# Optimization experiments

Measured on AMD Instinct MI355X. Metric: run time of the kernel, lower is better.

The kernel has to match this reference:

```python
import jax, jax.numpy as jnp
import numpy as np

B, T, D, H, DK, DV, C, M = 8, 512, 1024, 8, 128, 128, 512, 512
TAU = float(DK) ** 0.5

def _ln(x, g, b, eps=1e-6):
    mu = x.mean(-1, keepdims=True)
    var = ((x - mu) ** 2).mean(-1, keepdims=True)
    return (x - mu) * jax.lax.rsqrt(var + eps) * g + b

def _hln(x, eps=1e-6):
    mu = x.mean(-1, keepdims=True)
    var = ((x - mu) ** 2).mean(-1, keepdims=True)
    return (x - mu) * jax.lax.rsqrt(var + eps)

def setup_inputs() -> dict:
    key = jax.random.key(0)
    ks = jax.random.split(key, 14)
    s = lambda k, shape, fan: jax.random.normal(k, shape, jnp.float32) * (fan ** -0.5)
    return {
        "x": jax.random.normal(ks[0], (B, T, D), jnp.float32),
        "doc_ids": jax.random.randint(ks[1], (B, T), 0, 4),
        "loss_mask": jnp.ones((B, T), jnp.float32),
        "xl_k_hat": jax.random.normal(ks[2], (B, H, M, DK), jnp.float32),
        "xl_v": jax.random.normal(ks[3], (B, H, M, DV), jnp.float32),
        "agg_upper": jax.random.normal(ks[4], (B, H, C, DV), jnp.float32),
        "agg_lower": jax.random.uniform(ks[5], (B, H, C), jnp.float32) * 8.0,
        "w_ln_g": jnp.ones((D,), jnp.float32),
        "w_ln_b": jnp.zeros((D,), jnp.float32),
        "w_q": s(ks[6], (D, H * DK), D),
        "w_k": s(ks[7], (D, H * DK), D),
        "w_v": s(ks[8], (D, H * DV), D),
        "w_g": s(ks[9], (D, H * DV), D),
        "w_res": s(ks[10], (H * DV, D), H * DV),
        "x_u": jax.random.normal(ks[11], (H, DK), jnp.float32) * 0.02,
        "codebook": jax.random.normal(ks[12], (H, C, DK), jnp.float32),
    }

def reference(x, doc_ids, loss_mask, xl_k_hat, xl_v, agg_upper, agg_lower,
              w_ln_g, w_ln_b, w_q, w_k, w_v, w_g, w_res, x_u, codebook):
    # ---- compute_k_q_v_g ----
    xt = _ln(x, w_ln_g, w_ln_b)                                  # [B,T,D]
    q = _hln((xt @ w_q).reshape(B, T, H, DK).transpose(0, 2, 1, 3))  # [B,H,T,DK]
    k = _hln((xt @ w_k).reshape(B, T, H, DK).transpose(0, 2, 1, 3))  # [B,H,T,DK]
    v = (xt @ w_v).reshape(B, T, H, DV).transpose(0, 2, 1, 3)        # [B,H,T,DV]
    g = jax.nn.silu(xt @ w_g)                                        # [B,T,H*DV]

    # ---- vector quantize keys (LearnableVQ) ----
    # dist[b,h,t,c] = ||k - codebook||^2 ; argmin -> shortcodes z
    kc = jnp.einsum('bhtd,hcd->bhtc', k, codebook)
    dist = (k ** 2).sum(-1)[..., None] - 2.0 * kc + (codebook ** 2).sum(-1)[None, :, None, :]
    z = jnp.argmin(dist, axis=-1)                                 # [B,H,T] shortcodes
    k_hat = codebook[jnp.arange(H)[None, :, None], z]             # [B,H,T,DK]
    k_hat_st = k + jax.lax.stop_gradient(k_hat - k)               # straight-through
    mask = loss_mask[:, None, :]                                  # [B,1,T]
    denom_m = mask.sum() * H + 1e-6
    l_commit = (((k - jax.lax.stop_gradient(k_hat)) ** 2).sum(-1) * mask).sum() / denom_m
    l_codebook = (((jax.lax.stop_gradient(k) - k_hat) ** 2).sum(-1) * mask).sum() / denom_m

    # ---- attention over xlcache ++ present, plus aggregated codeword cache ----
    recent_k = jnp.concatenate([xl_k_hat, k_hat_st], axis=2)      # [B,H,M+T,DK]
    recent_v = jnp.concatenate([xl_v, v], axis=2)                 # [B,H,M+T,DV]
    qb = q + x_u[None, :, None, :]
    s_rec = jnp.einsum('bhtd,bhsd->bhts', qb, recent_k) / TAU     # [B,H,T,M+T]
    s_agg = jnp.einsum('bhtd,hcd->bhtc', qb, codebook) / TAU      # [B,H,T,C]

    i = jnp.arange(T)[:, None]
    j = jnp.arange(M + T)[None, :]
    allow = ((j - M) <= i).astype(s_rec.dtype)                    # causal over recent window
    NEG = jnp.asarray(-1e30, s_rec.dtype)
    s_rec_m = jnp.where(allow > 0, s_rec, NEG)

    m = jnp.maximum(s_rec_m.max(-1), s_agg.max(-1))               # [B,H,T]
    a_rec = jnp.exp(s_rec_m - m[..., None]) * allow               # [B,H,T,M+T]
    a_agg = jnp.exp(s_agg - m[..., None])                         # [B,H,T,C]
    den = a_rec.sum(-1) + jnp.einsum('bhtc,bhc->bht', a_agg, agg_lower)
    num = (jnp.einsum('bhts,bhsd->bhtd', a_rec, recent_v)
           + jnp.einsum('bhtc,bhcd->bhtd', a_agg, agg_upper))
    wv = num / den[..., None]                                     # [B,H,T,DV]

    o = wv.transpose(0, 2, 1, 3).reshape(B, T, H * DV) * g        # gated
    res = o @ w_res                                               # [B,T,D]
    return res, l_commit, l_codebook
```

## Files before the change

kernel.cpp:

```cpp
#include <hip/hip_runtime.h>
#include <math.h>

namespace {

constexpr int nB = 8, nT = 512, nD = 1024, nH = 8, nDK = 128, nDV = 128, nC = 512, nM = 512;
constexpr int NROW = nB * nT;
constexpr float RTAU = 0.08838834764831845f;

typedef __attribute__((ext_vector_type(8))) short short8;
typedef __attribute__((ext_vector_type(4))) float f32x4;

__device__ __forceinline__ ushort f2bf(float f) {
  union { float f; uint u; } x; x.f = f;
  uint r = x.u + 0x7fff + ((x.u >> 16) & 1);
  return (ushort)(r >> 16);
}
__device__ __forceinline__ uint pk2(float a, float b) {
  return (uint)f2bf(a) | ((uint)f2bf(b) << 16);
}
__device__ __forceinline__ float bf2f(ushort u) {
  return __uint_as_float(((uint)u) << 16);
}
__device__ __forceinline__ void gload16(const void* g, void* l) {
  __builtin_amdgcn_global_load_lds((const __attribute__((address_space(1))) void*)g,
                                   (__attribute__((address_space(3))) void*)l, 16, 0, 0);
}

__device__ __forceinline__ float blockReduce256(float v, float* sm) {
  int lane = threadIdx.x & 63, w = threadIdx.x >> 6;
#pragma unroll
  for (int off = 32; off; off >>= 1) v += __shfl_down(v, off);
  if (lane == 0) sm[w] = v;
  __syncthreads();
  float r = sm[0] + sm[1] + sm[2] + sm[3];
  __syncthreads();
  return r;
}

__global__ __launch_bounds__(256) void ln_kernel(const float* __restrict__ x,
                                                 const float* __restrict__ gw,
                                                 const float* __restrict__ bw,
                                                 ushort* __restrict__ xt_bf) {
  __shared__ float sm[4];
  size_t row = blockIdx.x;
  float4 v = ((const float4*)(x + row * nD))[threadIdx.x];
  float mu = blockReduce256(v.x + v.y + v.z + v.w, sm) * (1.f / nD);
  float4 d = make_float4(v.x - mu, v.y - mu, v.z - mu, v.w - mu);
  float var = blockReduce256(d.x * d.x + d.y * d.y + d.z * d.z + d.w * d.w, sm) * (1.f / nD);
  float rs = rsqrtf(var + 1e-6f);
  float4 gg = ((const float4*)gw)[threadIdx.x];
  float4 bb = ((const float4*)bw)[threadIdx.x];
  float4 o = make_float4(d.x * rs * gg.x + bb.x, d.y * rs * gg.y + bb.y,
                         d.z * rs * gg.z + bb.z, d.w * rs * gg.w + bb.w);
  uint2 pb;
  pb.x = pk2(o.x, o.y);
  pb.y = pk2(o.z, o.w);
  ((uint2*)(xt_bf + row * nD))[threadIdx.x] = pb;
}

__global__ __launch_bounds__(256) void tobf3_kernel(const float* __restrict__ s0,
                                                    ushort* __restrict__ d0,
                                                    const float* __restrict__ s1,
                                                    ushort* __restrict__ d1,
                                                    const float* __restrict__ s2,
                                                    ushort* __restrict__ d2) {
  const float* src = blockIdx.y == 0 ? s0 : (blockIdx.y == 1 ? s1 : s2);
  ushort* dst = blockIdx.y == 0 ? d0 : (blockIdx.y == 1 ? d1 : d2);
  size_t i = (size_t)blockIdx.x * 256 + threadIdx.x;
  float4 v = ((const float4*)src)[i];
  uint2 p;
  p.x = pk2(v.x, v.y);
  p.y = pk2(v.z, v.w);
  ((uint2*)dst)[i] = p;
}

__global__ __launch_bounds__(256) void wtrans_kernel(const float* __restrict__ wq,
                                                     const float* __restrict__ wk,
                                                     const float* __restrict__ wv,
                                                     const float* __restrict__ wg,
                                                     const float* __restrict__ wres,
                                                     ushort* __restrict__ wqkvg_t,
                                                     ushort* __restrict__ wres_t) {
  __shared__ float tile[64][65];
  const int kz = blockIdx.x * 64;
  const int nz = blockIdx.y * 64;
  const float* W;
  ushort* D;
  if (blockIdx.z == 0)      { W = wq;   D = wqkvg_t; }
  else if (blockIdx.z == 1) { W = wk;   D = wqkvg_t + (size_t)1024 * 1024; }
  else if (blockIdx.z == 2) { W = wv;   D = wqkvg_t + (size_t)2048 * 1024; }
  else if (blockIdx.z == 3) { W = wg;   D = wqkvg_t + (size_t)3072 * 1024; }
  else                      { W = wres; D = wres_t; }
  const int c = threadIdx.x & 63, r4 = threadIdx.x >> 6;
#pragma unroll
  for (int i = 0; i < 16; ++i) {
    int r = i * 4 + r4;
    tile[r][c] = W[(size_t)(kz + r) * 1024 + nz + c];
  }
  __syncthreads();
#pragma unroll
  for (int i = 0; i < 16; ++i) {
    int n = i * 4 + r4;
    D[(size_t)(nz + n) * 1024 + kz + c] = f2bf(tile[c][n]);
  }
}

template <int MODE>
__global__ __launch_bounds__(256) void gemm_bf16_kernel(const ushort* __restrict__ A,
                                                        const ushort* __restrict__ Bt,
                                                        float* __restrict__ C0,
                                                        ushort* __restrict__ C1,
                                                        ushort* __restrict__ C2,
                                                        ushort* __restrict__ C3) {
  __shared__ __align__(16) ushort As[128 * 32];
  __shared__ __align__(16) ushort Bs[128 * 32];
  const int tid = threadIdx.x;
  const int w = tid >> 6, l = tid & 63;
  const int lr = l & 15, lg = l >> 4;
  const int wr = w >> 1, wc = w & 1;
  const int n0 = blockIdx.x * 128;
  const int m0 = blockIdx.y * 128;
  constexpr int K = 1024;

  f32x4 acc[4][4];
#pragma unroll
  for (int i = 0; i < 4; ++i)
#pragma unroll
    for (int j = 0; j < 4; ++j) acc[i][j] = (f32x4){0.f, 0.f, 0.f, 0.f};

  const int e0 = w * 512 + l * 8;
  const int r0 = e0 >> 5, c0 = e0 & 31;
  const int e1 = 2048 + e0;
  const int r1 = e1 >> 5, c1 = e1 & 31;
  const ushort* a0p = A + (size_t)(m0 + r0) * K + c0;
  const ushort* a1p = A + (size_t)(m0 + r1) * K + c1;
  const ushort* b0p = Bt + (size_t)(n0 + r0) * K + c0;
  const ushort* b1p = Bt + (size_t)(n0 + r1) * K + c1;
  ushort* lA0 = &As[w * 512];
  ushort* lA1 = &As[2048 + w * 512];
  ushort* lB0 = &Bs[w * 512];
  ushort* lB1 = &Bs[2048 + w * 512];

  for (int k0 = 0; k0 < K; k0 += 32) {
    __syncthreads();
    gload16(a0p + k0, lA0);
    gload16(a1p + k0, lA1);
    gload16(b0p + k0, lB0);
    gload16(b1p + k0, lB1);
    __syncthreads();
    short8 af[4], bfr[4];
#pragma unroll
    for (int i = 0; i < 4; ++i) af[i] = *(const short8*)&As[(wr * 64 + i * 16 + lr) * 32 + lg * 8];
#pragma unroll
    for (int j = 0; j < 4; ++j) bfr[j] = *(const short8*)&Bs[(wc * 64 + j * 16 + lr) * 32 + lg * 8];
    __builtin_amdgcn_s_setprio(1);
#pragma unroll
    for (int i = 0; i < 4; ++i)
#pragma unroll
      for (int j = 0; j < 4; ++j)
        acc[i][j] = __builtin_amdgcn_mfma_f32_16x16x32_bf16(af[i], bfr[j], acc[i][j], 0, 0, 0);
    __builtin_amdgcn_s_setprio(0);
  }

  const int seg = n0 >> 10;
  const int nbase = n0 & 1023;
#pragma unroll
  for (int i = 0; i < 4; ++i)
#pragma unroll
    for (int j = 0; j < 4; ++j)
#pragma unroll
      for (int r2 = 0; r2 < 4; ++r2) {
        const int row = m0 + wr * 64 + i * 16 + lg * 4 + r2;
        const int col = wc * 64 + j * 16 + lr;
        float v = acc[i][j][r2];
        if (MODE == 0) {
          C0[(size_t)row * 1024 + n0 + col] = v;
        } else {
          const int nloc = nbase + col;
          if (seg == 0)      C1[(size_t)row * 1024 + nloc] = f2bf(v);
          else if (seg == 1) C0[(size_t)row * 1024 + nloc] = v;
          else if (seg == 2) C2[(size_t)row * 1024 + nloc] = f2bf(v);
          else {
            float s = v / (1.f + __expf(-v));
            C3[(size_t)row * 1024 + nloc] = f2bf(s);
          }
        }
      }
}

__global__ __launch_bounds__(256) void hln_kernel(float* __restrict__ buf,
                                                  ushort* __restrict__ kbf,
                                                  float* __restrict__ knorm2) {
  int lane = threadIdx.x & 63;
  size_t row = (size_t)blockIdx.x * 4 + (threadIdx.x >> 6);
  float* p = buf + row * 128;
  float2 v = *(float2*)(p + lane * 2);
  float s = v.x + v.y;
#pragma unroll
  for (int off = 32; off; off >>= 1) s += __shfl_down(s, off);
  float mu = __shfl(s, 0) * (1.f / 128.f);
  float dx = v.x - mu, dy = v.y - mu;
  float q = dx * dx + dy * dy;
#pragma unroll
  for (int off = 32; off; off >>= 1) q += __shfl_down(q, off);
  float qf = __shfl(q, 0);
  float rs = rsqrtf(qf * (1.f / 128.f) + 1e-6f);
  float ox = dx * rs, oy = dy * rs;
  *(float2*)(p + lane * 2) = make_float2(ox, oy);
  *(uint*)(kbf + row * 128 + lane * 2) = pk2(ox, oy);
  if (lane == 0) knorm2[row] = qf * rs * rs;
}

__global__ __launch_bounds__(256) void hln_bf_kernel(ushort* __restrict__ buf,
                                                     const float* __restrict__ xu) {
  int lane = threadIdx.x & 63;
  size_t row = (size_t)blockIdx.x * 4 + (threadIdx.x >> 6);
  ushort* p = buf + row * 128;
  uint u = *(uint*)(p + lane * 2);
  float vx = bf2f((ushort)(u & 0xffff)), vy = bf2f((ushort)(u >> 16));
  float s = vx + vy;
#pragma unroll
  for (int off = 32; off; off >>= 1) s += __shfl_down(s, off);
  float mu = __shfl(s, 0) * (1.f / 128.f);
  float dx = vx - mu, dy = vy - mu;
  float q = dx * dx + dy * dy;
#pragma unroll
  for (int off = 32; off; off >>= 1) q += __shfl_down(q, off);
  float rs = rsqrtf(__shfl(q, 0) * (1.f / 128.f) + 1e-6f);
  int h = (int)(row & 7);
  float ox = dx * rs + xu[h * 128 + lane * 2];
  float oy = dy * rs + xu[h * 128 + lane * 2 + 1];
  *(uint*)(p + lane * 2) = pk2(ox, oy);
}

__global__ __launch_bounds__(128) void cbprep_kernel(const float* __restrict__ cb,
                                                     float* __restrict__ cbn,
                                                     ushort* __restrict__ cb_bf) {
  __shared__ float sm[2];
  const int hc = blockIdx.x;
  float v = cb[(size_t)hc * 128 + threadIdx.x];
  cb_bf[(size_t)hc * 128 + threadIdx.x] = f2bf(v);
  float s = v * v;
#pragma unroll
  for (int off = 32; off; off >>= 1) s += __shfl_down(s, off);
  if ((threadIdx.x & 63) == 0) sm[threadIdx.x >> 6] = s;
  __syncthreads();
  if (threadIdx.x == 0) cbn[hc] = sm[0] + sm[1];
}

__global__ __launch_bounds__(256) void vq_mfma_kernel(const ushort* __restrict__ kbf,
                                                      const ushort* __restrict__ cb_bf,
                                                      const float* __restrict__ cbn,
                                                      const float* __restrict__ knorm2,
                                                      const float* __restrict__ mask,
                                                      ushort* __restrict__ khat_bf,
                                                      float* __restrict__ blocksq) {
  __shared__ ushort Kb[64][136];
  __shared__ ushort Cb[64][136];
  __shared__ float cnsh[64];
  __shared__ int zsh[64];
  __shared__ float dsh[64];
  const int tid = threadIdx.x;
  const int w = tid >> 6, l = tid & 63;
  const int lr = l & 15, lg = l >> 4;
  const int b = blockIdx.y >> 3, h = blockIdx.y & 7;
  const int t0 = blockIdx.x * 64;
  const int srow = tid >> 2, sd = (tid & 3) * 32;

  {
    const ushort* src = kbf + ((size_t)((b * nT + t0 + srow) * nH + h)) * 128 + sd;
    *(uint4*)&Kb[srow][sd] = *(const uint4*)src;
    *(uint4*)&Kb[srow][sd + 8] = *(const uint4*)(src + 8);
    *(uint4*)&Kb[srow][sd + 16] = *(const uint4*)(src + 16);
    *(uint4*)&Kb[srow][sd + 24] = *(const uint4*)(src + 24);
  }
  __syncthreads();

  short8 af[4];
#pragma unroll
  for (int k0 = 0; k0 < 4; ++k0) af[k0] = *(const short8*)&Kb[w * 16 + lr][k0 * 32 + lg * 8];

  float best[4] = {1e30f, 1e30f, 1e30f, 1e30f};
  int bidx[4] = {0, 0, 0, 0};

  for (int cc = 0; cc < 8; ++cc) {
    __syncthreads();
    {
      const ushort* src = cb_bf + ((size_t)(h * nC + cc * 64 + srow)) * 128 + sd;
      *(uint4*)&Cb[srow][sd] = *(const uint4*)src;
      *(uint4*)&Cb[srow][sd + 8] = *(const uint4*)(src + 8);
      *(uint4*)&Cb[srow][sd + 16] = *(const uint4*)(src + 16);
      *(uint4*)&Cb[srow][sd + 24] = *(const uint4*)(src + 24);
      if (tid < 64) cnsh[tid] = cbn[h * nC + cc * 64 + tid];
    }
    __syncthreads();
#pragma unroll
    for (int ct = 0; ct < 4; ++ct) {
      f32x4 z = (f32x4){0.f, 0.f, 0.f, 0.f};
#pragma unroll
      for (int k0 = 0; k0 < 4; ++k0) {
        short8 cf = *(const short8*)&Cb[ct * 16 + lr][k0 * 32 + lg * 8];
        z = __builtin_amdgcn_mfma_f32_16x16x32_bf16(af[k0], cf, z, 0, 0, 0);
      }
      const int code = cc * 64 + ct * 16 + lr;
      const float cn = cnsh[ct * 16 + lr];
#pragma unroll
      for (int r2 = 0; r2 < 4; ++r2) {
        float d = cn - 2.f * z[r2];
        if (d < best[r2]) { best[r2] = d; bidx[r2] = code; }
      }
    }
  }

#pragma unroll
  for (int off = 1; off < 16; off <<= 1) {
#pragma unroll
    for (int r2 = 0; r2 < 4; ++r2) {
      float od = __shfl_xor(best[r2], off);
      int oi = __shfl_xor(bidx[r2], off);
      if (od < best[r2] || (od == best[r2] && oi < bidx[r2])) { best[r2] = od; bidx[r2] = oi; }
    }
  }
  if (lr == 0) {
#pragma unroll
    for (int r2 = 0; r2 < 4; ++r2) {
      int row = w * 16 + lg * 4 + r2;
      zsh[row] = bidx[r2];
      dsh[row] = best[r2];
    }
  }
  __syncthreads();

  {
    const int row = tid >> 2, part = (tid & 3) * 32;
    const ushort* src = cb_bf + ((size_t)(h * nC + zsh[row])) * 128 + part;
    ushort* dst = khat_bf + ((size_t)((b * nT + t0 + row) * nH + h)) * 128 + part;
    *(uint4*)dst = *(const uint4*)src;
    *(uint4*)(dst + 8) = *(const uint4*)(src + 8);
    *(uint4*)(dst + 16) = *(const uint4*)(src + 16);
    *(uint4*)(dst + 24) = *(const uint4*)(src + 24);
  }

  if (tid < 64) {
    float s = mask[b * nT + t0 + tid] *
              (knorm2[(size_t)(b * nT + t0 + tid) * nH + h] + dsh[tid]);
#pragma unroll
    for (int off = 32; off; off >>= 1) s += __shfl_down(s, off);
    if (tid == 0) blocksq[blockIdx.y * gridDim.x + blockIdx.x] = s;
  }
}

__global__ __launch_bounds__(256) void attn_mfma_kernel(
    const ushort* __restrict__ qb, const ushort* __restrict__ khat,
    const ushort* __restrict__ vbuf, const ushort* __restrict__ xlk,
    const ushort* __restrict__ xlv, const ushort* __restrict__ cbb,
    const ushort* __restrict__ aggU, const float* __restrict__ aggL,
    const ushort* __restrict__ gbuf, ushort* __restrict__ o) {
  __shared__ ushort Ks[64][136];
  __shared__ ushort Vts[128][72];
  __shared__ ushort Ps[4][16][72];
  __shared__ float lowb[64];

  const int tid = threadIdx.x;
  const int w = tid >> 6, l = tid & 63;
  const int lr = l & 15, lg = l >> 4;
  const int b = blockIdx.x >> 3, h = blockIdx.x & 7;
  const int t0 = blockIdx.y * 64;

  short8 qf[4];
  {
    const ushort* qrow = qb + ((size_t)((b * nT + t0 + w * 16 + lr) * nH + h)) * 128;
#pragma unroll
    for (int k0 = 0; k0 < 4; ++k0) qf[k0] = *(const short8*)(qrow + k0 * 32 + lg * 8);
  }

  float m_r[4] = {-1e30f, -1e30f, -1e30f, -1e30f};
  float l_r[4] = {0.f, 0.f, 0.f, 0.f};
  f32x4 acc_o[8];
#pragma unroll
  for (int dt = 0; dt < 8; ++dt) acc_o[dt] = (f32x4){0.f, 0.f, 0.f, 0.f};

  const int srow = tid >> 2, sd = (tid & 3) * 32;
  const int kp = tid & 31, dbase = (tid >> 5) * 16;

  auto stageK = [&](const ushort* src) {
#pragma unroll
    for (int q4 = 0; q4 < 4; ++q4)
      *(uint4*)&Ks[srow][sd + q4 * 8] = *(const uint4*)(src + q4 * 8);
  };
  auto stageVbf = [&](const ushort* v0, const ushort* v1) {
    short8 a0 = *(const short8*)(v0);
    short8 a1 = *(const short8*)(v0 + 8);
    short8 b0 = *(const short8*)(v1);
    short8 b1 = *(const short8*)(v1 + 8);
#pragma unroll
    for (int i2 = 0; i2 < 8; ++i2) {
      *(uint*)&Vts[dbase + i2][2 * kp] = (uint)(ushort)a0[i2] | ((uint)(ushort)b0[i2] << 16);
      *(uint*)&Vts[dbase + 8 + i2][2 * kp] = (uint)(ushort)a1[i2] | ((uint)(ushort)b1[i2] << 16);
    }
  };

  auto chunk_body = [&](int sbase, bool AGG, bool MASKQ) {
    f32x4 sc[4];
    __builtin_amdgcn_s_setprio(1);
#pragma unroll
    for (int kt = 0; kt < 4; ++kt) {
      f32x4 z = (f32x4){0.f, 0.f, 0.f, 0.f};
#pragma unroll
      for (int k0 = 0; k0 < 4; ++k0) {
        short8 kf = *(const short8*)&Ks[kt * 16 + lr][k0 * 32 + lg * 8];
        z = __builtin_amdgcn_mfma_f32_16x16x32_bf16(qf[k0], kf, z, 0, 0, 0);
      }
      sc[kt] = z;
    }
    __builtin_amdgcn_s_setprio(0);
    float sv[4][4];
    float pm[4] = {-1e30f, -1e30f, -1e30f, -1e30f};
#pragma unroll
    for (int kt = 0; kt < 4; ++kt)
#pragma unroll
      for (int r2 = 0; r2 < 4; ++r2) {
        float s = sc[kt][r2] * RTAU;
        if (MASKQ) {
          int key = sbase + kt * 16 + lr;
          int tl = t0 + w * 16 + lg * 4 + r2 + nM;
          if (key > tl) s = -1e30f;
        }
        sv[kt][r2] = s;
        pm[r2] = fmaxf(pm[r2], s);
      }
#pragma unroll
    for (int r2 = 0; r2 < 4; ++r2)
#pragma unroll
      for (int off = 1; off < 16; off <<= 1) pm[r2] = fmaxf(pm[r2], __shfl_xor(pm[r2], off));
    float scale[4], rs[4];
#pragma unroll
    for (int r2 = 0; r2 < 4; ++r2) {
      float mn = fmaxf(m_r[r2], pm[r2]);
      scale[r2] = __expf(m_r[r2] - mn);
      m_r[r2] = mn;
      rs[r2] = 0.f;
    }
#pragma unroll
    for (int kt = 0; kt < 4; ++kt)
#pragma unroll
      for (int r2 = 0; r2 < 4; ++r2) {
        float p = __expf(sv[kt][r2] - m_r[r2]);
        rs[r2] += AGG ? p * lowb[kt * 16 + lr] : p;
        Ps[w][lg * 4 + r2][kt * 16 + lr] = f2bf(p);
      }
#pragma unroll
    for (int r2 = 0; r2 < 4; ++r2)
#pragma unroll
      for (int off = 1; off < 16; off <<= 1) rs[r2] += __shfl_xor(rs[r2], off);
#pragma unroll
    for (int r2 = 0; r2 < 4; ++r2) l_r[r2] = l_r[r2] * scale[r2] + rs[r2];
#pragma unroll
    for (int dt = 0; dt < 8; ++dt)
#pragma unroll
      for (int r2 = 0; r2 < 4; ++r2) acc_o[dt][r2] *= scale[r2];
    short8 pa0 = *(const short8*)&Ps[w][lr][lg * 8];
    short8 pa1 = *(const short8*)&Ps[w][lr][32 + lg * 8];
    __builtin_amdgcn_s_setprio(1);
#pragma unroll
    for (int dt = 0; dt < 8; ++dt) {
      short8 vf0 = *(const short8*)&Vts[dt * 16 + lr][lg * 8];
      short8 vf1 = *(const short8*)&Vts[dt * 16 + lr][32 + lg * 8];
      acc_o[dt] = __builtin_amdgcn_mfma_f32_16x16x32_bf16(pa0, vf0, acc_o[dt], 0, 0, 0);
      acc_o[dt] = __builtin_amdgcn_mfma_f32_16x16x32_bf16(pa1, vf1, acc_o[dt], 0, 0, 0);
    }
    __builtin_amdgcn_s_setprio(0);
  };

  const int nch = t0 / 64 + 9;
  for (int ci = 0; ci < nch; ++ci) {
    const int sbase = ci * 64;
    __syncthreads();
    {
      int s = sbase + srow;
      const ushort* src = (s < nM)
          ? xlk + ((size_t)(b * nH + h) * nM + s) * 128 + sd
          : khat + ((size_t)((b * nT + (s - nM)) * nH + h)) * 128 + sd;
      stageK(src);
    }
    {
      int s0 = sbase + 2 * kp;
      if (s0 < nM) {
        const ushort* v0 = xlv + ((size_t)(b * nH + h) * nM + s0) * 128 + dbase;
        stageVbf(v0, v0 + 128);
      } else {
        const ushort* v0 = vbuf + ((size_t)((b * nT + (s0 - nM)) * nH + h)) * 128 + dbase;
        stageVbf(v0, v0 + nH * 128);
      }
    }
    __syncthreads();
    chunk_body(sbase, false, ci == nch - 1);
  }

  for (int ca = 0; ca < 8; ++ca) {
    const int sbase = ca * 64;
    __syncthreads();
    stageK(cbb + ((size_t)h * nC + sbase + srow) * 128 + sd);
    {
      const ushort* v0 = aggU + ((size_t)(b * nH + h) * nC + sbase + 2 * kp) * 128 + dbase;
      stageVbf(v0, v0 + 128);
    }
    if (tid < 64) lowb[tid] = aggL[(size_t)(b * nH + h) * nC + sbase + tid];
    __syncthreads();
    chunk_body(sbase, true, false);
  }

  float inv[4];
#pragma unroll
  for (int r2 = 0; r2 < 4; ++r2) inv[r2] = 1.f / l_r[r2];
#pragma unroll
  for (int dt = 0; dt < 8; ++dt)
#pragma unroll
    for (int r2 = 0; r2 < 4; ++r2) {
      int trow = t0 + w * 16 + lg * 4 + r2;
      size_t oi = ((size_t)(b * nT + trow)) * nD + h * 128 + dt * 16 + lr;
      float gv = bf2f(gbuf[oi]);
      o[oi] = f2bf(acc_o[dt][r2] * inv[r2] * gv);
    }
}

__global__ __launch_bounds__(256) void finalize_kernel(const float* __restrict__ blocksq,
                                                       int nblk,
                                                       const float* __restrict__ mask,
                                                       float* __restrict__ outp) {
  __shared__ float sm[8];
  const int tid = threadIdx.x;
  float s = 0.f, ms = 0.f;
  for (int i = tid; i < NROW; i += 256) {
    if (i < nblk) s += blocksq[i];
    ms += mask[i];
  }
#pragma unroll
  for (int off = 32; off; off >>= 1) { s += __shfl_down(s, off); ms += __shfl_down(ms, off); }
  if ((tid & 63) == 0) { sm[tid >> 6] = s; sm[4 + (tid >> 6)] = ms; }
  __syncthreads();
  if (tid == 0) {
    float ts = sm[0] + sm[1] + sm[2] + sm[3];
    float tm = sm[4] + sm[5] + sm[6] + sm[7];
    float l = ts / (tm * (float)nH + 1e-6f);
    outp[0] = l;
    outp[1] = l;
  }
}

}

extern "C" void kernel_launch(void* const* d_in, const int* in_sizes, int n_in,
                              void* d_out, int out_size, void* d_ws, size_t ws_size,
                              hipStream_t stream) {
  const float* x    = (const float*)d_in[0];
  const float* mask = (const float*)d_in[2];
  const float* xlk  = (const float*)d_in[3];
  const float* xlv  = (const float*)d_in[4];
  const float* aggU = (const float*)d_in[5];
  const float* aggL = (const float*)d_in[6];
  const float* wlng = (const float*)d_in[7];
  const float* wlnb = (const float*)d_in[8];
  const float* wq   = (const float*)d_in[9];
  const float* wk   = (const float*)d_in[10];
  const float* wv   = (const float*)d_in[11];
  const float* wg   = (const float*)d_in[12];
  const float* wres = (const float*)d_in[13];
  const float* xu   = (const float*)d_in[14];
  const float* cb   = (const float*)d_in[15];
  float* out = (float*)d_out;

  float* ws = (float*)d_ws;
  const size_t SZ = (size_t)NROW * nD;
  float*  kbuf    = ws;
  ushort* qbuf_bf = (ushort*)(ws + SZ);
  ushort* khat_bf = (ushort*)(ws + SZ + SZ / 2);
  ushort* vbuf_bf = (ushort*)(ws + 2 * SZ);
  ushort* gbuf_bf = (ushort*)(ws + 2 * SZ + SZ / 2);
  ushort* xt_bf   = (ushort*)(ws + 3 * SZ);
  ushort* wqkvg_t = (ushort*)(ws + 3 * SZ + SZ / 2);
  ushort* wres_t  = (ushort*)(ws + 4 * SZ);
  ushort* xlk_bf  = (ushort*)(ws + 4 * SZ + SZ / 8);
  ushort* xlv_bf  = (ushort*)(ws + 4 * SZ + SZ / 8 + SZ / 2);
  ushort* aggU_bf = (ushort*)(ws + 4 * SZ + SZ / 8 + SZ);
  ushort* cb_bf   = (ushort*)(ws + 4 * SZ + SZ / 8 + 3 * SZ / 2);
  float*  cbn     = ws + 4 * SZ + SZ / 8 + 3 * SZ / 2 + SZ / 16;
  float*  knorm2  = cbn + 4096;
  float*  bsq     = knorm2 + 32768;
  ushort* kbf     = xt_bf;
  ushort* obuf_bf = xt_bf;

  ln_kernel<<<NROW, 256, 0, stream>>>(x, wlng, wlnb, xt_bf);
  wtrans_kernel<<<dim3(16, 16, 5), 256, 0, stream>>>(wq, wk, wv, wg, wres, wqkvg_t, wres_t);
  cbprep_kernel<<<nH * nC, 128, 0, stream>>>(cb, cbn, cb_bf);
  tobf3_kernel<<<dim3(4096, 3), 256, 0, stream>>>(xlk, xlk_bf, xlv, xlv_bf, aggU, aggU_bf);

  gemm_bf16_kernel<1><<<dim3(32, 32), 256, 0, stream>>>(xt_bf, wqkvg_t, kbuf,
                                                        qbuf_bf, vbuf_bf, gbuf_bf);

  hln_bf_kernel<<<(NROW * nH) / 4, 256, 0, stream>>>(qbuf_bf, xu);
  hln_kernel<<<(NROW * nH) / 4, 256, 0, stream>>>(kbuf, kbf, knorm2);

  vq_mfma_kernel<<<dim3(nT / 64, nB * nH), 256, 0, stream>>>(kbf, cb_bf, cbn, knorm2,
                                                             mask, khat_bf, bsq);

  attn_mfma_kernel<<<dim3(nB * nH, nT / 64), 256, 0, stream>>>(
      qbuf_bf, khat_bf, vbuf_bf, xlk_bf, xlv_bf, cb_bf, aggU_bf, aggL, gbuf_bf, obuf_bf);

  gemm_bf16_kernel<0><<<dim3(8, 32), 256, 0, stream>>>(obuf_bf, wres_t, out,
                                                       nullptr, nullptr, nullptr);
  finalize_kernel<<<1, 256, 0, stream>>>(bsq, nT / 64 * nB * nH, mask, out + SZ);
}
```

Baseline: 250.4 us.

## Prefetch next K/V chunk into registers in attention; merge headwise LN kernels

The attention kernel now loads the next chunk's K, V and aggregate-lower values into registers while the current chunk is computed, then writes them to LDS at the top of the next iteration. The recent-window and aggregate loops are merged into one loop. This hides global-load latency behind the MFMA work, at the cost of extra registers that may reduce occupancy. The two headwise LayerNorm kernels for q and k are also fused into one launch split on blockIdx.y, and the unused fp32 writeback of normalized k is dropped.

```diff
diff --git a/kernel.cpp b/kernel.cpp
--- a/kernel.cpp
+++ b/kernel.cpp
@@ -188,49 +188,47 @@
       }
 }
 
-__global__ __launch_bounds__(256) void hln_kernel(float* __restrict__ buf,
-                                                  ushort* __restrict__ kbf,
-                                                  float* __restrict__ knorm2) {
+__global__ __launch_bounds__(256) void hln_both_kernel(ushort* __restrict__ qbuf,
+                                                       const float* __restrict__ xu,
+                                                       float* __restrict__ kbuf,
+                                                       ushort* __restrict__ kbf,
+                                                       float* __restrict__ knorm2) {
   int lane = threadIdx.x & 63;
   size_t row = (size_t)blockIdx.x * 4 + (threadIdx.x >> 6);
-  float* p = buf + row * 128;
-  float2 v = *(float2*)(p + lane * 2);
-  float s = v.x + v.y;
-#pragma unroll
-  for (int off = 32; off; off >>= 1) s += __shfl_down(s, off);
-  float mu = __shfl(s, 0) * (1.f / 128.f);
-  float dx = v.x - mu, dy = v.y - mu;
-  float q = dx * dx + dy * dy;
-#pragma unroll
-  for (int off = 32; off; off >>= 1) q += __shfl_down(q, off);
-  float qf = __shfl(q, 0);
-  float rs = rsqrtf(qf * (1.f / 128.f) + 1e-6f);
-  float ox = dx * rs, oy = dy * rs;
-  *(float2*)(p + lane * 2) = make_float2(ox, oy);
-  *(uint*)(kbf + row * 128 + lane * 2) = pk2(ox, oy);
-  if (lane == 0) knorm2[row] = qf * rs * rs;
-}
-
-__global__ __launch_bounds__(256) void hln_bf_kernel(ushort* __restrict__ buf,
-                                                     const float* __restrict__ xu) {
-  int lane = threadIdx.x & 63;
-  size_t row = (size_t)blockIdx.x * 4 + (threadIdx.x >> 6);
-  ushort* p = buf + row * 128;
-  uint u = *(uint*)(p + lane * 2);
-  float vx = bf2f((ushort)(u & 0xffff)), vy = bf2f((ushort)(u >> 16));
-  float s = vx + vy;
-#pragma unroll
-  for (int off = 32; off; off >>= 1) s += __shfl_down(s, off);
-  float mu = __shfl(s, 0) * (1.f / 128.f);
-  float dx = vx - mu, dy = vy - mu;
-  float q = dx * dx + dy * dy;
-#pragma unroll
-  for (int off = 32; off; off >>= 1) q += __shfl_down(q, off);
-  float rs = rsqrtf(__shfl(q, 0) * (1.f / 128.f) + 1e-6f);
-  int h = (int)(row & 7);
-  float ox = dx * rs + xu[h * 128 + lane * 2];
-  float oy = dy * rs + xu[h * 128 + lane * 2 + 1];
-  *(uint*)(p + lane * 2) = pk2(ox, oy);
+  if (blockIdx.y == 0) {
+    ushort* p = qbuf + row * 128;
+    uint u = *(uint*)(p + lane * 2);
+    float vx = bf2f((ushort)(u & 0xffff)), vy = bf2f((ushort)(u >> 16));
+    float s = vx + vy;
+#pragma unroll
+    for (int off = 32; off; off >>= 1) s += __shfl_down(s, off);
+    float mu = __shfl(s, 0) * (1.f / 128.f);
+    float dx = vx - mu, dy = vy - mu;
+    float q = dx * dx + dy * dy;
+#pragma unroll
+    for (int off = 32; off; off >>= 1) q += __shfl_down(q, off);
+    float rs = rsqrtf(__shfl(q, 0) * (1.f / 128.f) + 1e-6f);
+    int h = (int)(row & 7);
+    float ox = dx * rs + xu[h * 128 + lane * 2];
+    float oy = dy * rs + xu[h * 128 + lane * 2 + 1];
+    *(uint*)(p + lane * 2) = pk2(ox, oy);
+  } else {
+    float* p = kbuf + row * 128;
+    float2 v = *(float2*)(p + lane * 2);
+    float s = v.x + v.y;
+#pragma unroll
+    for (int off = 32; off; off >>= 1) s += __shfl_down(s, off);
+    float mu = __shfl(s, 0) * (1.f / 128.f);
+    float dx = v.x - mu, dy = v.y - mu;
+    float q = dx * dx + dy * dy;
+#pragma unroll
+    for (int off = 32; off; off >>= 1) q += __shfl_down(q, off);
+    float qf = __shfl(q, 0);
+    float rs = rsqrtf(qf * (1.f / 128.f) + 1e-6f);
+    float ox = dx * rs, oy = dy * rs;
+    *(uint*)(kbf + row * 128 + lane * 2) = pk2(ox, oy);
+    if (lane == 0) knorm2[row] = qf * rs * rs;
+  }
 }
 
 __global__ __launch_bounds__(128) void cbprep_kernel(const float* __restrict__ cb,
@@ -383,21 +381,57 @@
   const int srow = tid >> 2, sd = (tid & 3) * 32;
   const int kp = tid & 31, dbase = (tid >> 5) * 16;
 
-  auto stageK = [&](const ushort* src) {
-#pragma unroll
-    for (int q4 = 0; q4 < 4; ++q4)
-      *(uint4*)&Ks[srow][sd + q4 * 8] = *(const uint4*)(src + q4 * 8);
+  const int nch = t0 / 64 + 9;
+  const int ntot = nch + 8;
+
+  uint4 kreg[4];
+  short8 va0, va1, vb0, vb1;
+  float lowreg = 0.f;
+
+  auto loadRegs = [&](int ci) {
+    if (ci < nch) {
+      const int s = ci * 64 + srow;
+      const ushort* srcK = (s < nM)
+          ? xlk + ((size_t)(b * nH + h) * nM + s) * 128 + sd
+          : khat + ((size_t)((b * nT + (s - nM)) * nH + h)) * 128 + sd;
+#pragma unroll
+      for (int q4 = 0; q4 < 4; ++q4) kreg[q4] = *(const uint4*)(srcK + q4 * 8);
+      const int s0 = ci * 64 + 2 * kp;
+      const ushort *v0, *v1;
+      if (s0 < nM) {
+        v0 = xlv + ((size_t)(b * nH + h) * nM + s0) * 128 + dbase;
+        v1 = v0 + 128;
+      } else {
+        v0 = vbuf + ((size_t)((b * nT + (s0 - nM)) * nH + h)) * 128 + dbase;
+        v1 = v0 + nH * 128;
+      }
+      va0 = *(const short8*)(v0);
+      va1 = *(const short8*)(v0 + 8);
+      vb0 = *(const short8*)(v1);
+      vb1 = *(const short8*)(v1 + 8);
+    } else {
+      const int sbase = (ci - nch) * 64;
+      const ushort* srcK = cbb + ((size_t)(h * nC + sbase + srow)) * 128 + sd;
+#pragma unroll
+      for (int q4 = 0; q4 < 4; ++q4) kreg[q4] = *(const uint4*)(srcK + q4 * 8);
+      const ushort* v0 = aggU + ((size_t)(b * nH + h) * nC + sbase + 2 * kp) * 128 + dbase;
+      va0 = *(const short8*)(v0);
+      va1 = *(const short8*)(v0 + 8);
+      vb0 = *(const short8*)(v0 + 128);
+      vb1 = *(const short8*)(v0 + 136);
+      if (tid < 64) lowreg = aggL[(size_t)(b * nH + h) * nC + sbase + tid];
+    }
   };
-  auto stageVbf = [&](const ushort* v0, const ushort* v1) {
-    short8 a0 = *(const short8*)(v0);
-    short8 a1 = *(const short8*)(v0 + 8);
-    short8 b0 = *(const short8*)(v1);
-    short8 b1 = *(const short8*)(v1 + 8);
+
+  auto writeLDS = [&](bool isAgg) {
+#pragma unroll
+    for (int q4 = 0; q4 < 4; ++q4) *(uint4*)&Ks[srow][sd + q4 * 8] = kreg[q4];
 #pragma unroll
     for (int i2 = 0; i2 < 8; ++i2) {
-      *(uint*)&Vts[dbase + i2][2 * kp] = (uint)(ushort)a0[i2] | ((uint)(ushort)b0[i2] << 16);
-      *(uint*)&Vts[dbase + 8 + i2][2 * kp] = (uint)(ushort)a1[i2] | ((uint)(ushort)b1[i2] << 16);
-    }
+      *(uint*)&Vts[dbase + i2][2 * kp] = (uint)(ushort)va0[i2] | ((uint)(ushort)vb0[i2] << 16);
+      *(uint*)&Vts[dbase + 8 + i2][2 * kp] = (uint)(ushort)va1[i2] | ((uint)(ushort)vb1[i2] << 16);
+    }
+    if (isAgg && tid < 64) lowb[tid] = lowreg;
   };
 
   auto chunk_body = [&](int sbase, bool AGG, bool MASKQ) {
@@ -472,42 +506,15 @@
     __builtin_amdgcn_s_setprio(0);
   };
 
-  const int nch = t0 / 64 + 9;
-  for (int ci = 0; ci < nch; ++ci) {
-    const int sbase = ci * 64;
+  loadRegs(0);
+  for (int ci = 0; ci < ntot; ++ci) {
+    const bool isAgg = ci >= nch;
+    writeLDS(isAgg);
     __syncthreads();
-    {
-      int s = sbase + srow;
-      const ushort* src = (s < nM)
-          ? xlk + ((size_t)(b * nH + h) * nM + s) * 128 + sd
-          : khat + ((size_t)((b * nT + (s - nM)) * nH + h)) * 128 + sd;
-      stageK(src);
-    }
-    {
-      int s0 = sbase + 2 * kp;
-      if (s0 < nM) {
-        const ushort* v0 = xlv + ((size_t)(b * nH + h) * nM + s0) * 128 + dbase;
-        stageVbf(v0, v0 + 128);
-      } else {
-        const ushort* v0 = vbuf + ((size_t)((b * nT + (s0 - nM)) * nH + h)) * 128 + dbase;
-        stageVbf(v0, v0 + nH * 128);
-      }
-    }
+    if (ci + 1 < ntot) loadRegs(ci + 1);
+    const int sbase = isAgg ? (ci - nch) * 64 : ci * 64;
+    chunk_body(sbase, isAgg, ci == nch - 1);
     __syncthreads();
-    chunk_body(sbase, false, ci == nch - 1);
-  }
-
-  for (int ca = 0; ca < 8; ++ca) {
-    const int sbase = ca * 64;
-    __syncthreads();
-    stageK(cbb + ((size_t)h * nC + sbase + srow) * 128 + sd);
-    {
-      const ushort* v0 = aggU + ((size_t)(b * nH + h) * nC + sbase + 2 * kp) * 128 + dbase;
-      stageVbf(v0, v0 + 128);
-    }
-    if (tid < 64) lowb[tid] = aggL[(size_t)(b * nH + h) * nC + sbase + tid];
-    __syncthreads();
-    chunk_body(sbase, true, false);
   }
 
   float inv[4];
@@ -598,8 +605,8 @@
   gemm_bf16_kernel<1><<<dim3(32, 32), 256, 0, stream>>>(xt_bf, wqkvg_t, kbuf,
                                                         qbuf_bf, vbuf_bf, gbuf_bf);
 
-  hln_bf_kernel<<<(NROW * nH) / 4, 256, 0, stream>>>(qbuf_bf, xu);
-  hln_kernel<<<(NROW * nH) / 4, 256, 0, stream>>>(kbuf, kbf, knorm2);
+  hln_both_kernel<<<dim3((NROW * nH) / 4, 2), 256, 0, stream>>>(qbuf_bf, xu,
+                                                                kbuf, kbf, knorm2);
 
   vq_mfma_kernel<<<dim3(nT / 64, nB * nH), 256, 0, stream>>>(kbf, cb_bf, cbn, knorm2,
                                                              mask, khat_bf, bsq);
```

New measurement: 270.0 us. 1.08x slower.
